# Kernel tuning notes

Measured on AMD Instinct MI355X. Metric: run time of the kernel, lower is better.

The kernel has to match this reference:

```python
import jax, jax.numpy as jnp
import numpy as np

B, T, D = 4, 2048, 2048
H, G, HD = 16, 4, 128
NB, BS = 512, 16  # num_blocks, block_size
GS = H // G
SCALE = HD ** -0.5
NEG = -1e30


def setup_inputs() -> dict:
    key = jax.random.key(0)
    ks = jax.random.split(key, 5)
    x = jax.random.normal(ks[0], (B, T, D), dtype=jnp.float32)
    block_tables = jnp.arange(B * (T // BS), dtype=jnp.int32).reshape(B, T // BS)
    kv_lens = jnp.zeros((B,), dtype=jnp.int32)
    k_blocks = jnp.zeros((NB, G, BS, HD), jnp.float32)
    v_blocks = jnp.zeros((NB, G, BS, HD), jnp.float32)
    w_q = jax.random.normal(ks[1], (D, H * HD), jnp.float32) * 0.02
    w_k = jax.random.normal(ks[2], (D, G * HD), jnp.float32) * 0.02
    w_v = jax.random.normal(ks[3], (D, G * HD), jnp.float32) * 0.02
    w_o = jax.random.normal(ks[4], (H * HD, D), jnp.float32) * 0.02
    return {"x": x, "w_q": w_q, "w_k": w_k, "w_v": w_v, "w_o": w_o,
            "k_blocks": k_blocks, "v_blocks": v_blocks,
            "block_tables": block_tables, "kv_lens": kv_lens}


def reference(x, w_q, w_k, w_v, w_o, k_blocks, v_blocks, block_tables, kv_lens):
    # projections
    q = (x @ w_q).reshape(B, T, H, HD).transpose(0, 2, 1, 3)   # [B,H,T,Hd]
    k = (x @ w_k).reshape(B, T, G, HD).transpose(0, 2, 1, 3)   # [B,G,T,Hd]
    v = (x @ w_v).reshape(B, T, G, HD).transpose(0, 2, 1, 3)

    # paged cache append (vectorized scatter over [B,T])
    pos = kv_lens[:, None] + jnp.arange(T)                     # [B,T]
    slot, off = pos // BS, pos % BS
    bid = jnp.take_along_axis(block_tables, slot, axis=1)      # [B,T] block ids
    k_blocks = k_blocks.at[bid, :, off, :].set(k.transpose(0, 2, 1, 3))
    v_blocks = v_blocks.at[bid, :, off, :].set(v.transpose(0, 2, 1, 3))

    # gather contiguous KV per request; prefill: kv_lens == 0 -> seq_len = T
    S = T
    nb = (S + BS - 1) // BS
    blk = block_tables[:, :nb]                                 # [B,nb]
    k_seq = k_blocks[blk].transpose(0, 2, 1, 3, 4).reshape(B, G, nb * BS, HD)[:, :, :S]
    v_seq = v_blocks[blk].transpose(0, 2, 1, 3, 4).reshape(B, G, nb * BS, HD)[:, :, :S]

    # original's flat reshapes pair head h with kv group (h % G)
    qg = q.reshape(B, GS, G, T, HD)
    scores = jnp.einsum('bjgqd,bgkd->bjgqk', qg, k_seq) * SCALE

    q_pos = (S - T) + jnp.arange(T)
    k_pos = jnp.arange(S)
    causal = k_pos[None, :] <= q_pos[:, None]                  # [T,S]
    scores = jnp.where(causal, scores, NEG)
    attn = jax.nn.softmax(scores, axis=-1)

    out = jnp.einsum('bjgqk,bgkd->bjgqd', attn, v_seq)         # [B,GS,G,T,Hd]
    out = out.reshape(B, H, T, HD).transpose(0, 2, 1, 3).reshape(B, T, H * HD)
    return out @ w_o
```

## Files before the change

kernel.cpp:

```cpp
#include <hip/hip_runtime.h>
#include <stdint.h>

typedef __attribute__((ext_vector_type(8))) short short8;
typedef __attribute__((ext_vector_type(8))) unsigned short ushort8;
typedef __attribute__((ext_vector_type(4))) float f32x4;

__device__ __forceinline__ ushort f2bf(float f) {
  union { float f; uint32_t u; } v; v.f = f;
  uint32_t r = v.u + 0x7FFFu + ((v.u >> 16) & 1u);
  return (ushort)(r >> 16);
}

__device__ __forceinline__ ushort f2bf_trunc(float f) {
  union { float f; uint32_t u; } v; v.f = f;
  return (ushort)(v.u >> 16);
}

__device__ __forceinline__ float fexp2(float x) {
  float r;
  asm("v_exp_f32 %0, %1" : "=v"(r) : "v"(x));
  return r;
}

__device__ __forceinline__ void gld16(const ushort* g, ushort* l) {
  __builtin_amdgcn_global_load_lds((const __attribute__((address_space(1))) void*)g,
                                   (__attribute__((address_space(3))) void*)l, 16, 0, 0);
}

__global__ __launch_bounds__(256) void k_f32_to_bf16(const float* __restrict__ in,
                                                     ushort* __restrict__ out, long n) {
  long i = ((long)blockIdx.x * 256 + threadIdx.x) * 8;
  if (i >= n) return;
  float4 a = *(const float4*)(in + i);
  float4 b = *(const float4*)(in + i + 4);
  ushort8 o;
  o[0] = f2bf(a.x); o[1] = f2bf(a.y); o[2] = f2bf(a.z); o[3] = f2bf(a.w);
  o[4] = f2bf(b.x); o[5] = f2bf(b.y); o[6] = f2bf(b.z); o[7] = f2bf(b.w);
  *(ushort8*)(out + i) = o;
}

__global__ __launch_bounds__(256) void k_w_transpose(const float* __restrict__ in,
                                                     ushort* __restrict__ out, int R, int C) {
  __shared__ float t[32][33];
  int tx = threadIdx.x & 31, ty = threadIdx.x >> 5;
  int r0 = blockIdx.y * 32, c0 = blockIdx.x * 32;
#pragma unroll
  for (int i = 0; i < 4; i++)
    t[ty + i * 8][tx] = in[(size_t)(r0 + ty + i * 8) * C + c0 + tx];
  __syncthreads();
#pragma unroll
  for (int i = 0; i < 4; i++)
    out[(size_t)(c0 + ty + i * 8) * R + r0 + tx] = f2bf(t[tx][ty + i * 8]);
}

__global__ __launch_bounds__(256) void k_v_transpose(const ushort* __restrict__ qkv,
                                                     ushort* __restrict__ out) {
  __shared__ ushort t[32][33];
  int tx = threadIdx.x & 31, ty = threadIdx.x >> 5;
  int t0 = blockIdx.x * 32, d0 = blockIdx.y * 32;
  int b = blockIdx.z >> 2, g = blockIdx.z & 3;
#pragma unroll
  for (int i = 0; i < 4; i++)
    t[ty + i * 8][tx] =
        qkv[((size_t)b * 2048 + t0 + ty + i * 8) * 3072 + 2560 + g * 128 + d0 + tx];
  __syncthreads();
#pragma unroll
  for (int i = 0; i < 4; i++)
    out[(((size_t)b * 4 + g) * 128 + d0 + ty + i * 8) * 2048 + t0 + tx] = t[tx][ty + i * 8];
}

template <int NCH8>
__device__ __forceinline__ void stageT(const ushort* G, int ldg, ushort* Ls, int tid) {
  int l = tid & 63, w = tid >> 6;
  int rsub = l >> 3;
  int cs = ((l & 7) ^ rsub) << 3;
#pragma unroll
  for (int n = 0; n < NCH8; n++) {
    int c = n * 8 + w;
    gld16(G + (size_t)(c * 8 + rsub) * ldg + cs, Ls + c * 512 + l * 8);
  }
}

template <int F32OUT, int NF>
__global__ __launch_bounds__(512) void k_gemm256(const ushort* __restrict__ A,
                                                 const ushort* __restrict__ BT,
                                                 void* __restrict__ C, int M, int N, int K) {
  constexpr int BN = NF * 64;
  __shared__ ushort As0[256 * 64], As1[256 * 64];
  __shared__ ushort Bs0[BN * 64], Bs1[BN * 64];
  const int tid = threadIdx.x;
  const int lane = tid & 63, wid = tid >> 6;
  const int wm = wid >> 2, wn = wid & 3;
  const int l15 = lane & 15, l4 = lane >> 4;
  const int rsw = (l15 & 7) << 3;
  int nwg = gridDim.x * gridDim.y;
  int lin = blockIdx.y * gridDim.x + blockIdx.x;
  int swz = (lin & 7) * (nwg >> 3) + (lin >> 3);
  int bx = swz % gridDim.x, by = swz / gridDim.x;
  const int m0 = by * 256, n0 = bx * BN;

  const ushort* Atile = A + (size_t)m0 * K;
  const ushort* Btile = BT + (size_t)n0 * K;
  const int NK = K >> 6;

  f32x4 acc[8][NF] = {};

  stageT<4>(Atile, K, As0, tid);
  stageT<NF>(Btile, K, Bs0, tid);
  stageT<4>(Atile + 64, K, As1, tid);
  stageT<NF>(Btile + 64, K, Bs1, tid);
  if constexpr (NF == 4) asm volatile("s_waitcnt vmcnt(8)" ::: "memory");
  else                   asm volatile("s_waitcnt vmcnt(7)" ::: "memory");
  asm volatile("s_barrier" ::: "memory");

  for (int kt = 0; kt < NK; ++kt) {
    const ushort* Ab = (kt & 1) ? As1 : As0;
    const ushort* Bb = (kt & 1) ? Bs1 : Bs0;
    short8 bfrag[NF][2];
#pragma unroll
    for (int nf = 0; nf < NF; nf++)
#pragma unroll
      for (int ks = 0; ks < 2; ks++)
        bfrag[nf][ks] = *(const short8*)&Bb[(wn * (NF * 16) + nf * 16 + l15) * 64 +
                                            ((ks * 32 + l4 * 8) ^ rsw)];
#pragma unroll
    for (int q = 0; q < 4; q++) {
      short8 afr[2][2];
#pragma unroll
      for (int dm = 0; dm < 2; dm++)
#pragma unroll
        for (int ks = 0; ks < 2; ks++)
          afr[dm][ks] = *(const short8*)&Ab[(wm * 128 + (q * 2 + dm) * 16 + l15) * 64 +
                                            ((ks * 32 + l4 * 8) ^ rsw)];
      __builtin_amdgcn_s_setprio(1);
#pragma unroll
      for (int dm = 0; dm < 2; dm++)
#pragma unroll
        for (int nf = 0; nf < NF; nf++)
#pragma unroll
          for (int ks = 0; ks < 2; ks++)
            acc[q * 2 + dm][nf] = __builtin_amdgcn_mfma_f32_16x16x32_bf16(
                afr[dm][ks], bfrag[nf][ks], acc[q * 2 + dm][nf], 0, 0, 0);
      __builtin_amdgcn_s_setprio(0);
    }
    asm volatile("s_barrier" ::: "memory");
    if (kt + 2 < NK) {
      stageT<4>(Atile + (kt + 2) * 64, K, (kt & 1) ? As1 : As0, tid);
      stageT<NF>(Btile + (kt + 2) * 64, K, (kt & 1) ? Bs1 : Bs0, tid);
      if constexpr (NF == 4) asm volatile("s_waitcnt vmcnt(8)" ::: "memory");
      else                   asm volatile("s_waitcnt vmcnt(7)" ::: "memory");
    } else {
      asm volatile("s_waitcnt vmcnt(0)" ::: "memory");
    }
    asm volatile("s_barrier" ::: "memory");
  }

#pragma unroll
  for (int mf = 0; mf < 8; mf++)
#pragma unroll
    for (int nf = 0; nf < NF; nf++)
#pragma unroll
      for (int r = 0; r < 4; r++) {
        int m = m0 + wm * 128 + mf * 16 + l4 * 4 + r;
        int n = n0 + wn * (NF * 16) + nf * 16 + l15;
        if (F32OUT)
          ((float*)C)[(size_t)m * N + n] = acc[mf][nf][r];
        else
          ((ushort*)C)[(size_t)m * N + n] = f2bf(acc[mf][nf][r]);
      }
}

__device__ __forceinline__ void stage_k8(const ushort* Kt, ushort* Ks, int tid) {
  int l = tid & 63, w = tid >> 6;
#pragma unroll
  for (int n = 0; n < 2; n++) {
    int cidx = w * 2 + n;
    int r = cidx * 4 + (l >> 4);
    int cs = ((l & 15) * 8) ^ ((r & 7) << 3);
    gld16(Kt + (size_t)r * 3072 + cs, Ks + cidx * 512 + l * 8);
  }
}

__device__ __forceinline__ void stage_v8(const ushort* Vt, ushort* Vs, int tid) {
  int l = tid & 63, w = tid >> 6;
#pragma unroll
  for (int n = 0; n < 2; n++) {
    int cidx = w * 2 + n;
    int d = cidx * 8 + (l >> 3);
    int cs = ((l & 7) * 8) ^ ((d & 7) << 3);
    gld16(Vt + (size_t)d * 2048 + cs, Vs + cidx * 512 + l * 8);
  }
}

__global__ __launch_bounds__(512) void k_attn(const ushort* __restrict__ QKV,
                                              const ushort* __restrict__ VT,
                                              ushort* __restrict__ O) {
  const int T = 2048, HD = 128, G = 4, H = 16, RS = 3072;
  const float SCALE2 = 0.08838834764831845f * 1.4426950408889634f;
  const float MFIX = 12.0f;
  int bid = blockIdx.x;
  int pr = bid >> 6;
  int bh = bid & 63;
  int h = bh & 15, b = bh >> 4;
  int g = h & 3;
  int tid = threadIdx.x, wid = tid >> 6, lane = tid & 63;
  int l15 = lane & 15, l4 = lane >> 4;
  int kswz = (l15 & 7) << 3;

  __shared__ __align__(16) char smem[102400];
  ushort* Ks0 = (ushort*)smem;
  ushort* Ks1 = (ushort*)(smem + 16384);
  ushort* Vs0 = (ushort*)(smem + 32768);
  ushort* Vs1 = (ushort*)(smem + 49152);
  ushort* Pw  = (ushort*)(smem + 65536) + wid * (32 * 72);

  const ushort* Qb = &QKV[(size_t)b * T * RS + h * HD];
  const ushort* Kb = &QKV[(size_t)b * T * RS + 2048 + g * HD];
  const ushort* Vb = &VT[((size_t)b * G + g) * (size_t)HD * T];

#pragma unroll 1
  for (int half = 0; half < 2; half++) {
    int ch = half ? pr : (7 - pr);
    int qw = ch * 256 + wid * 32;
    int nt = 4 * (ch + 1);

    short8 qf[2][4];
#pragma unroll
    for (int mf = 0; mf < 2; mf++)
#pragma unroll
      for (int kf = 0; kf < 4; kf++)
        qf[mf][kf] = *(const short8*)&Qb[(size_t)(qw + mf * 16 + l15) * RS + kf * 32 + l4 * 8];

    f32x4 o[2][8] = {};
    float lrow[8];
#pragma unroll
    for (int i = 0; i < 8; i++) lrow[i] = 0.f;

    stage_k8(Kb, Ks0, tid);
    stage_v8(Vb, Vs0, tid);
    __syncthreads();

#pragma unroll 1
    for (int it = 0; it < nt; ++it) {
      int t0 = it * 64;
      int cur = it & 1;
      ushort* Kc = cur ? Ks1 : Ks0;
      ushort* Vc = cur ? Vs1 : Vs0;
      if (it + 1 < nt) {
        stage_k8(Kb + (size_t)(t0 + 64) * RS, cur ? Ks0 : Ks1, tid);
        stage_v8(Vb + t0 + 64, cur ? Vs0 : Vs1, tid);
      }
      if (t0 <= qw + 31) {
        f32x4 s[2][4] = {};
#pragma unroll
        for (int kf = 0; kf < 4; kf++) {
#pragma unroll
          for (int nf = 0; nf < 4; nf++) {
            short8 bk = *(const short8*)&Kc[(nf * 16 + l15) * 128 + ((kf * 32 + l4 * 8) ^ kswz)];
            s[0][nf] = __builtin_amdgcn_mfma_f32_16x16x32_bf16(qf[0][kf], bk, s[0][nf], 0, 0, 0);
            s[1][nf] = __builtin_amdgcn_mfma_f32_16x16x32_bf16(qf[1][kf], bk, s[1][nf], 0, 0, 0);
          }
        }
        bool needmask = (t0 + 63 > qw);
        if (needmask) {
#pragma unroll
          for (int mf = 0; mf < 2; mf++)
#pragma unroll
            for (int nf = 0; nf < 4; nf++)
#pragma unroll
              for (int r = 0; r < 4; r++) {
                int qq = qw + mf * 16 + l4 * 4 + r;
                int kk = t0 + nf * 16 + l15;
                if (kk > qq) s[mf][nf][r] = -1e30f;
              }
        }
        float rs[8];
#pragma unroll
        for (int i = 0; i < 8; i++) rs[i] = 0.f;
#pragma unroll
        for (int mf = 0; mf < 2; mf++)
#pragma unroll
          for (int nf = 0; nf < 4; nf++)
#pragma unroll
            for (int r = 0; r < 4; r++) {
              float pq = fexp2(__builtin_fmaf(s[mf][nf][r], SCALE2, -MFIX));
              rs[mf * 4 + r] += pq;
              Pw[(mf * 16 + l4 * 4 + r) * 72 + nf * 16 + l15] = f2bf_trunc(pq);
            }
#pragma unroll
        for (int i = 0; i < 8; i++) lrow[i] += rs[i];
#pragma unroll
        for (int kf = 0; kf < 2; kf++) {
          short8 pa0 = *(const short8*)&Pw[(l15) * 72 + kf * 32 + l4 * 8];
          short8 pa1 = *(const short8*)&Pw[(16 + l15) * 72 + kf * 32 + l4 * 8];
#pragma unroll
          for (int nfo = 0; nfo < 8; nfo++) {
            short8 bv = *(const short8*)&Vc[(nfo * 16 + l15) * 64 + ((kf * 32 + l4 * 8) ^ kswz)];
            o[0][nfo] = __builtin_amdgcn_mfma_f32_16x16x32_bf16(pa0, bv, o[0][nfo], 0, 0, 0);
            o[1][nfo] = __builtin_amdgcn_mfma_f32_16x16x32_bf16(pa1, bv, o[1][nfo], 0, 0, 0);
          }
        }
      }
      __syncthreads();
    }

#pragma unroll
    for (int i = 0; i < 8; i++) {
      float x = lrow[i];
      x += __shfl_xor(x, 1);
      x += __shfl_xor(x, 2);
      x += __shfl_xor(x, 4);
      x += __shfl_xor(x, 8);
      lrow[i] = x;
    }
    float inv[8];
#pragma unroll
    for (int i = 0; i < 8; i++) inv[i] = 1.0f / lrow[i];
#pragma unroll
    for (int mf = 0; mf < 2; mf++)
#pragma unroll
      for (int nfo = 0; nfo < 8; nfo++)
#pragma unroll
        for (int r = 0; r < 4; r++) {
          int t = qw + mf * 16 + l4 * 4 + r;
          int d = nfo * 16 + l15;
          O[(((size_t)b * T + t) * H + h) * HD + d] = f2bf(o[mf][nfo][r] * inv[mf * 4 + r]);
        }
    __syncthreads();
  }
}

extern "C" void kernel_launch(void* const* d_in, const int* in_sizes, int n_in,
                              void* d_out, int out_size, void* d_ws, size_t ws_size,
                              hipStream_t stream) {
  const float* x   = (const float*)d_in[0];
  const float* w_q = (const float*)d_in[1];
  const float* w_k = (const float*)d_in[2];
  const float* w_v = (const float*)d_in[3];
  const float* w_o = (const float*)d_in[4];

  char* ws = (char*)d_ws;
  ushort* xbf  = (ushort*)(ws);
  ushort* wkvT = (ushort*)(ws + 33554432ul);
  ushort* woT  = (ushort*)(ws + 46137344ul);
  ushort* qkvb = (ushort*)(ws + 54525952ul);
  ushort* VTb  = (ushort*)(ws + 104857600ul);
  ushort* attn = xbf;

  k_f32_to_bf16<<<8192, 256, 0, stream>>>(x, xbf, 16777216L);
  k_w_transpose<<<dim3(64, 64), 256, 0, stream>>>(w_q, wkvT, 2048, 2048);
  k_w_transpose<<<dim3(16, 64), 256, 0, stream>>>(w_k, wkvT + 2048ul * 2048, 2048, 512);
  k_w_transpose<<<dim3(16, 64), 256, 0, stream>>>(w_v, wkvT + 2560ul * 2048, 2048, 512);
  k_w_transpose<<<dim3(64, 64), 256, 0, stream>>>(w_o, woT, 2048, 2048);

  k_gemm256<0, 3><<<dim3(16, 32), 512, 0, stream>>>(xbf, wkvT, qkvb, 8192, 3072, 2048);

  k_v_transpose<<<dim3(64, 4, 16), 256, 0, stream>>>(qkvb, VTb);

  k_attn<<<256, 512, 0, stream>>>(qkvb, VTb, attn);

  k_gemm256<1, 4><<<dim3(8, 32), 512, 0, stream>>>(attn, woT, (float*)d_out, 8192, 2048, 2048);
}
```

Measured before the change: 312.7 us.

## Add 256x192 GEMM with triple-buffered A and staggered staging for QKV projection

Adds a new GEMM kernel for the QKV projection that uses a 256x192 output tile with a 3-deep A buffer and 2-deep B buffer in shared memory. Global-to-LDS loads for step t+2 are spread across the four MFMA sub-phases, and s_setprio raises priority around the MFMA bursts. The goal is to hide load latency and keep matrix cores busy. The cost is heavier LDS use (about 144KB) and extra barriers per K-step, which may lower occupancy or add sync overhead. The grid shape stays the same because 3072/192 = 16 column tiles.

```diff
diff --git a/kernel.cpp b/kernel.cpp
--- a/kernel.cpp
+++ b/kernel.cpp
@@ -170,6 +170,146 @@
       }
 }
 
+__device__ __forceinline__ void stageA_half(const ushort* Atile, int K, int t,
+                                            ushort* slot, int h, int tid) {
+#pragma unroll
+  for (int n = 0; n < 2; n++) {
+    int row = h * 128 + n * 64 + (tid >> 3);
+    int c0 = (tid & 7) * 8;
+    int cs = c0 ^ ((row & 7) << 3);
+    gld16(Atile + (size_t)row * K + t * 64 + cs, slot + row * 64 + c0);
+  }
+}
+
+__device__ __forceinline__ void stageB_third(const ushort* Btile, int K, int t,
+                                             ushort* slot, int b, int tid) {
+  int row = b * 64 + (tid >> 3);
+  int c0 = (tid & 7) * 8;
+  int cs = c0 ^ ((row & 7) << 3);
+  gld16(Btile + (size_t)row * K + t * 64 + cs, slot + row * 64 + c0);
+}
+
+__global__ __launch_bounds__(512) void k_gemm192p(const ushort* __restrict__ A,
+                                                  const ushort* __restrict__ BT,
+                                                  ushort* __restrict__ C, int M, int N, int K) {
+  __shared__ ushort As[3][16384];
+  __shared__ ushort Bs[2][12288];
+  const int tid = threadIdx.x;
+  const int lane = tid & 63, wid = tid >> 6;
+  const int wm = wid >> 2, wn = wid & 3;
+  const int l15 = lane & 15, l4 = lane >> 4;
+  const int rsw = (l15 & 7) << 3;
+  int nwg = gridDim.x * gridDim.y;
+  int lin = blockIdx.y * gridDim.x + blockIdx.x;
+  int swz = (lin & 7) * (nwg >> 3) + (lin >> 3);
+  int bx = swz % gridDim.x, by = swz / gridDim.x;
+  const int m0 = by * 256, n0 = bx * 192;
+  const ushort* Atile = A + (size_t)m0 * K;
+  const ushort* Btile = BT + (size_t)n0 * K;
+  const int NK = K >> 6;
+
+  f32x4 acc[8][3] = {};
+
+  stageA_half(Atile, K, 0, As[0], 0, tid);
+  stageA_half(Atile, K, 0, As[0], 1, tid);
+  stageB_third(Btile, K, 0, Bs[0], 0, tid);
+  stageB_third(Btile, K, 0, Bs[0], 1, tid);
+  stageB_third(Btile, K, 0, Bs[0], 2, tid);
+  stageA_half(Atile, K, 1, As[1], 0, tid);
+  stageA_half(Atile, K, 1, As[1], 1, tid);
+  stageB_third(Btile, K, 1, Bs[1], 0, tid);
+  stageB_third(Btile, K, 1, Bs[1], 1, tid);
+  stageB_third(Btile, K, 1, Bs[1], 2, tid);
+  asm volatile("s_waitcnt vmcnt(7)" ::: "memory");
+  asm volatile("s_barrier" ::: "memory");
+
+#pragma unroll 1
+  for (int t = 0; t < NK; ++t) {
+    const ushort* Ab = As[t % 3];
+    const ushort* Bb = Bs[t & 1];
+    ushort* An = As[(t + 2) % 3];
+    ushort* Bn = Bs[t & 1];
+    const bool st = (t + 2 < NK);
+    short8 bfrag[3][2];
+
+#pragma unroll
+    for (int nf = 0; nf < 3; nf++)
+#pragma unroll
+      for (int ks = 0; ks < 2; ks++)
+        bfrag[nf][ks] = *(const short8*)&Bb[(wn * 48 + nf * 16 + l15) * 64 +
+                                            ((ks * 32 + l4 * 8) ^ rsw)];
+    {
+      short8 afr[2][2];
+#pragma unroll
+      for (int dm = 0; dm < 2; dm++)
+#pragma unroll
+        for (int ks = 0; ks < 2; ks++)
+          afr[dm][ks] = *(const short8*)&Ab[(wm * 128 + dm * 16 + l15) * 64 +
+                                            ((ks * 32 + l4 * 8) ^ rsw)];
+      if (st) stageA_half(Atile, K, t + 2, An, 0, tid);
+      asm volatile("s_barrier" ::: "memory");
+      __builtin_amdgcn_s_setprio(1);
+#pragma unroll
+      for (int dm = 0; dm < 2; dm++)
+#pragma unroll
+        for (int nf = 0; nf < 3; nf++)
+#pragma unroll
+          for (int ks = 0; ks < 2; ks++)
+            acc[dm][nf] = __builtin_amdgcn_mfma_f32_16x16x32_bf16(
+                afr[dm][ks], bfrag[nf][ks], acc[dm][nf], 0, 0, 0);
+      __builtin_amdgcn_s_setprio(0);
+      asm volatile("s_barrier" ::: "memory");
+    }
+#pragma unroll
+    for (int q = 1; q < 4; q++) {
+      short8 afr[2][2];
+#pragma unroll
+      for (int dm = 0; dm < 2; dm++)
+#pragma unroll
+        for (int ks = 0; ks < 2; ks++)
+          afr[dm][ks] = *(const short8*)&Ab[(wm * 128 + (q * 2 + dm) * 16 + l15) * 64 +
+                                            ((ks * 32 + l4 * 8) ^ rsw)];
+      if (st) {
+        if (q == 1) stageB_third(Btile, K, t + 2, Bn, 0, tid);
+        if (q == 2) stageB_third(Btile, K, t + 2, Bn, 1, tid);
+        if (q == 3) {
+          stageA_half(Atile, K, t + 2, An, 1, tid);
+          stageB_third(Btile, K, t + 2, Bn, 2, tid);
+        }
+      }
+      asm volatile("s_barrier" ::: "memory");
+      __builtin_amdgcn_s_setprio(1);
+#pragma unroll
+      for (int dm = 0; dm < 2; dm++)
+#pragma unroll
+        for (int nf = 0; nf < 3; nf++)
+#pragma unroll
+          for (int ks = 0; ks < 2; ks++)
+            acc[q * 2 + dm][nf] = __builtin_amdgcn_mfma_f32_16x16x32_bf16(
+                afr[dm][ks], bfrag[nf][ks], acc[q * 2 + dm][nf], 0, 0, 0);
+      __builtin_amdgcn_s_setprio(0);
+      if (q < 3) {
+        asm volatile("s_barrier" ::: "memory");
+      } else {
+        if (st) asm volatile("s_waitcnt vmcnt(7)" ::: "memory");
+        else    asm volatile("s_waitcnt vmcnt(0)" ::: "memory");
+        asm volatile("s_barrier" ::: "memory");
+      }
+    }
+  }
+
+#pragma unroll
+  for (int mf = 0; mf < 8; mf++)
+#pragma unroll
+    for (int nf = 0; nf < 3; nf++)
+#pragma unroll
+      for (int r = 0; r < 4; r++) {
+        int m = m0 + wm * 128 + mf * 16 + l4 * 4 + r;
+        int n = n0 + wn * 48 + nf * 16 + l15;
+        C[(size_t)m * N + n] = f2bf(acc[mf][nf][r]);
+      }
+}
+
 __device__ __forceinline__ void stage_k8(const ushort* Kt, ushort* Ks, int tid) {
   int l = tid & 63, w = tid >> 6;
 #pragma unroll
@@ -353,7 +493,7 @@
   k_w_transpose<<<dim3(16, 64), 256, 0, stream>>>(w_v, wkvT + 2560ul * 2048, 2048, 512);
   k_w_transpose<<<dim3(64, 64), 256, 0, stream>>>(w_o, woT, 2048, 2048);
 
-  k_gemm256<0, 3><<<dim3(16, 32), 512, 0, stream>>>(xbf, wkvT, qkvb, 8192, 3072, 2048);
+  k_gemm192p<<<dim3(16, 32), 512, 0, stream>>>(xbf, wkvT, qkvb, 8192, 3072, 2048);
 
   k_v_transpose<<<dim3(64, 4, 16), 256, 0, stream>>>(qkvb, VTb);
 
```

New measurement: 306.4 us (median of 2 runs). -2.0%, faster.
